# Kernel tuning notes

Hardware: AMD Instinct MI355X
Metric: run time of the kernel (lower is better)

Reference implementation:

```python
import jax, jax.numpy as jnp
import numpy as np

C = 512
GROUPS = 32
EPS = 1e-6


def setup_inputs() -> dict:
    key = jax.random.key(0)
    ks = jax.random.split(key, 6)
    B, L = 8, 2048
    x = jax.random.normal(ks[0], (B, C, L), dtype=jnp.float32)
    # fan_avg variance-scaling uniform for 1x1 conv weights [C, C]
    bound = float(np.sqrt(3.0 / C))  # fan_in == fan_out == C for 1x1 conv
    Wq = jax.random.uniform(ks[1], (C, C), jnp.float32, -bound, bound)
    Wk = jax.random.uniform(ks[2], (C, C), jnp.float32, -bound, bound)
    Wv = jax.random.uniform(ks[3], (C, C), jnp.float32, -bound, bound)
    # proj_out uses init_scale=0.0 (gain 1e-10) -> effectively zeros; use tiny
    bound0 = float(np.sqrt(3.0 * 1e-10 / C))
    Wp = jax.random.uniform(ks[4], (C, C), jnp.float32, -bound0, bound0)
    bq = jnp.zeros((C,), jnp.float32)
    bk = jnp.zeros((C,), jnp.float32)
    bv = jnp.zeros((C,), jnp.float32)
    bp = jnp.zeros((C,), jnp.float32)
    gamma = jnp.ones((C,), jnp.float32)
    beta = jnp.zeros((C,), jnp.float32)
    return {"x": x, "Wq": Wq, "bq": bq, "Wk": Wk, "bk": bk,
            "Wv": Wv, "bv": bv, "Wp": Wp, "bp": bp,
            "gamma": gamma, "beta": beta}


def _group_norm(x, gamma, beta):
    # x: [B, C, L]
    B, Cc, L = x.shape
    xg = x.reshape(B, GROUPS, Cc // GROUPS, L)
    mean = jnp.mean(xg, axis=(2, 3), keepdims=True)
    var = jnp.var(xg, axis=(2, 3), keepdims=True)
    xn = ((xg - mean) * jax.lax.rsqrt(var + EPS)).reshape(B, Cc, L)
    return xn * gamma[None, :, None] + beta[None, :, None]


def reference(x, Wq, bq, Wk, bk, Wv, bv, Wp, bp, gamma, beta):
    h = _group_norm(x, gamma, beta)
    # 1x1 convs are channel-mixing matmuls: out[b,o,l] = W[o,c] h[b,c,l] + b[o]
    q = jnp.einsum('oc,bcl->bol', Wq, h) + bq[None, :, None]
    k = jnp.einsum('oc,bcl->bol', Wk, h) + bk[None, :, None]
    v = jnp.einsum('oc,bcl->bol', Wv, h) + bv[None, :, None]
    scale = float(x.shape[1]) ** (-0.5)
    attn = jnp.einsum('bcl,bcm->blm', q, k) * scale  # [B, L, L]
    attn = jax.nn.softmax(attn, axis=-1)
    h2 = jnp.einsum('bcm,blm->bcl', v, attn)
    h2 = jnp.einsum('oc,bcl->bol', Wp, h2) + bp[None, :, None]
    return x + h2
```

## Files before the change

kernel.cpp:

```cpp
#include <hip/hip_runtime.h>
#include <cstdint>

#define B_DIM 8
#define C_DIM 512
#define L_DIM 2048
#define NGROUPS 32
#define CPG 16
#define EPSV 1e-6f

typedef unsigned short u16;
typedef unsigned int u32;
typedef __attribute__((ext_vector_type(4))) float f32x4;
typedef __attribute__((ext_vector_type(8))) short bf16x8;
typedef const __attribute__((address_space(1))) char gchar;
typedef __attribute__((address_space(3))) char lchar;

__device__ __forceinline__ u16 f2bf(float f) {
  u32 u = __float_as_uint(f);
  u = (u + 0x7fffu + ((u >> 16) & 1u)) >> 16;
  return (u16)u;
}
__device__ __forceinline__ float bf2f(u16 h) {
  return __uint_as_float(((u32)h) << 16);
}

__global__ __launch_bounds__(256) void f2bf_k(const float* __restrict__ in,
                                              u16* __restrict__ out, int n4) {
  int i = blockIdx.x * 256 + threadIdx.x;
  if (i >= n4) return;
  float4 v = ((const float4*)in)[i];
  int2 o;
  o.x = (int)((u32)f2bf(v.x) | ((u32)f2bf(v.y) << 16));
  o.y = (int)((u32)f2bf(v.z) | ((u32)f2bf(v.w) << 16));
  ((int2*)out)[i] = o;
}

__global__ __launch_bounds__(256) void bias_cat_k(const float* __restrict__ a,
                                                  const float* __restrict__ b,
                                                  float* __restrict__ o) {
  int i = blockIdx.x * 256 + threadIdx.x;
  if (i < C_DIM) o[i] = a[i];
  else if (i < 2 * C_DIM) o[i] = b[i - C_DIM];
}

__global__ __launch_bounds__(256) void gn_stats_k(const float* __restrict__ x,
                                                  float* __restrict__ meanp,
                                                  float* __restrict__ rstdp) {
  const int bg = blockIdx.x;
  const float4* xv = (const float4*)(x + (size_t)bg * CPG * L_DIM);
  const int tid = threadIdx.x;
  float s = 0.f, ss = 0.f;
  for (int i = tid; i < CPG * L_DIM / 4; i += 256) {
    float4 v = xv[i];
    s += v.x + v.y + v.z + v.w;
    ss += v.x * v.x + v.y * v.y + v.z * v.z + v.w * v.w;
  }
#pragma unroll
  for (int o = 32; o > 0; o >>= 1) {
    s += __shfl_down(s, o);
    ss += __shfl_down(ss, o);
  }
  __shared__ float r1[4], r2[4];
  if ((tid & 63) == 0) { r1[tid >> 6] = s; r2[tid >> 6] = ss; }
  __syncthreads();
  if (tid == 0) {
    float S = r1[0] + r1[1] + r1[2] + r1[3];
    float SS = r2[0] + r2[1] + r2[2] + r2[3];
    const float invn = 1.f / (CPG * L_DIM);
    float mu = S * invn;
    float var = SS * invn - mu * mu;
    meanp[bg] = mu;
    rstdp[bg] = rsqrtf(var + EPSV);
  }
}

__global__ __launch_bounds__(256) void gn_apply_k(
    const float* __restrict__ x, const float* __restrict__ meanp,
    const float* __restrict__ rstdp, const float* __restrict__ gamma,
    const float* __restrict__ beta, u16* __restrict__ hT) {
  __shared__ float sm[64][65];
  const int b = blockIdx.z, c0 = blockIdx.y * 64, l0 = blockIdx.x * 64;
  const int tid = threadIdx.x;
#pragma unroll
  for (int p = 0; p < 4; ++p) {
    int cc = p * 16 + (tid >> 4);
    int ll = (tid & 15) * 4;
    float4 v = *(const float4*)(x + ((size_t)b * C_DIM + c0 + cc) * L_DIM + l0 + ll);
    int grp = (c0 + cc) >> 4;
    float rs = rstdp[b * NGROUPS + grp];
    float ga = gamma[c0 + cc] * rs;
    float be = beta[c0 + cc] - meanp[b * NGROUPS + grp] * ga;
    sm[cc][ll + 0] = v.x * ga + be;
    sm[cc][ll + 1] = v.y * ga + be;
    sm[cc][ll + 2] = v.z * ga + be;
    sm[cc][ll + 3] = v.w * ga + be;
  }
  __syncthreads();
#pragma unroll
  for (int i = 0; i < 8; ++i) {
    int w = tid + 256 * i;
    int ll = w >> 5;
    int cw = (w & 31) * 2;
    u32 pk = (u32)f2bf(sm[cw][ll]) | ((u32)f2bf(sm[cw + 1][ll]) << 16);
    *(u32*)(hT + ((size_t)b * L_DIM + l0 + ll) * C_DIM + c0 + cw) = pk;
  }
}

__global__ __launch_bounds__(256) void softmax_k(u16* __restrict__ S) {
  const int tid = threadIdx.x;
  u16* row = S + (size_t)blockIdx.x * L_DIM;
  union { int4 v; u16 u[8]; } in;
  in.v = ((const int4*)row)[tid];
  float f[8];
#pragma unroll
  for (int j = 0; j < 8; ++j) f[j] = bf2f(in.u[j]);
  float mx = f[0];
#pragma unroll
  for (int j = 1; j < 8; ++j) mx = fmaxf(mx, f[j]);
#pragma unroll
  for (int o = 32; o > 0; o >>= 1) mx = fmaxf(mx, __shfl_down(mx, o));
  __shared__ float r1[4], r2[4];
  if ((tid & 63) == 0) r1[tid >> 6] = mx;
  __syncthreads();
  mx = fmaxf(fmaxf(r1[0], r1[1]), fmaxf(r1[2], r1[3]));
  float s = 0.f;
#pragma unroll
  for (int j = 0; j < 8; ++j) { f[j] = __expf(f[j] - mx); s += f[j]; }
#pragma unroll
  for (int o = 32; o > 0; o >>= 1) s += __shfl_down(s, o);
  if ((tid & 63) == 0) r2[tid >> 6] = s;
  __syncthreads();
  float inv = 1.f / (r2[0] + r2[1] + r2[2] + r2[3]);
  union { int4 v; u16 u[8]; } outp;
#pragma unroll
  for (int j = 0; j < 8; ++j) outp.u[j] = f2bf(f[j] * inv);
  ((int4*)row)[tid] = outp.v;
}

template <int MODE>
__global__ __launch_bounds__(256, 4) void gemm_tn(
    const u16* __restrict__ A, long sA, long lda,
    const u16* __restrict__ Bp, long sB, long ldb,
    void* __restrict__ Cv, long sC, int M, int N, int K,
    const float* __restrict__ bias, const float* __restrict__ Xres, long sX,
    float scale) {
  constexpr int BM = 128, BN = 128, BK = 64;
  __shared__ u16 smem[2 * BM * BK];
  u16* As = smem;
  u16* Bs = smem + BM * BK;
  const int bz = blockIdx.z;
  A += (long)bz * sA;
  Bp += (long)bz * sB;
  const int m0 = blockIdx.x * BM;
  const int n0 = blockIdx.y * BN;
  const int tid = threadIdx.x;
  const int lane = tid & 63;
  const int wid = tid >> 6;
  const int wr = wid >> 1, wc = wid & 1;

  f32x4 acc[4][4] = {};

  const int srow = wid * 32 + (lane >> 3);
  const int scolb = ((lane & 7) << 4) ^ (((lane >> 3) & 7) << 4);
  auto stage = [&](int k0) {
#pragma unroll
    for (int q = 0; q < 4; ++q) {
      int seg = wid * 4 + q;
      int row = srow + q * 8;
      const char* ga = (const char*)A + ((long)(m0 + row) * lda + k0) * 2 + scolb;
      __builtin_amdgcn_global_load_lds((gchar*)ga,
                                       (lchar*)((char*)As + seg * 1024), 16, 0, 0);
      const char* gb = (const char*)Bp + ((long)(n0 + row) * ldb + k0) * 2 + scolb;
      __builtin_amdgcn_global_load_lds((gchar*)gb,
                                       (lchar*)((char*)Bs + seg * 1024), 16, 0, 0);
    }
  };

  const int nkt = K / BK;
  stage(0);
  for (int kt = 0; kt < nkt; ++kt) {
    __syncthreads();
#pragma unroll
    for (int ks = 0; ks < 2; ++ks) {
      bf16x8 af[4], bfv[4];
#pragma unroll
      for (int f = 0; f < 4; ++f) {
        int ra = wr * 64 + f * 16 + (lane & 15);
        int oa = (ra * 128 + ks * 64 + ((lane >> 4) * 16)) ^ ((ra & 7) << 4);
        af[f] = *(const bf16x8*)((const char*)As + oa);
        int rb = wc * 64 + f * 16 + (lane & 15);
        int ob = (rb * 128 + ks * 64 + ((lane >> 4) * 16)) ^ ((rb & 7) << 4);
        bfv[f] = *(const bf16x8*)((const char*)Bs + ob);
      }
#pragma unroll
      for (int i = 0; i < 4; ++i)
#pragma unroll
        for (int j = 0; j < 4; ++j)
          acc[i][j] = __builtin_amdgcn_mfma_f32_16x16x32_bf16(af[i], bfv[j],
                                                              acc[i][j], 0, 0, 0);
    }
    if (kt + 1 < nkt) {
      __syncthreads();
      stage((kt + 1) * BK);
    }
  }

  const int mb = wr * 64 + ((lane >> 4) << 2);
  const int nb = wc * 64 + (lane & 15);
  if (MODE == 4) {
#pragma unroll
    for (int i = 0; i < 4; ++i)
#pragma unroll
      for (int j = 0; j < 4; ++j)
#pragma unroll
        for (int r = 0; r < 4; ++r) {
          int m = m0 + mb + i * 16 + r;
          int n = n0 + nb + j * 16;
          long off = (long)m * N + n;
          ((float*)Cv)[(long)bz * sC + off] =
              acc[i][j][r] + bias[m] + Xres[(long)bz * sX + off];
        }
  } else {
    __syncthreads();
    u16* Cs = smem;
#pragma unroll
    for (int i = 0; i < 4; ++i)
#pragma unroll
      for (int j = 0; j < 4; ++j)
#pragma unroll
        for (int r = 0; r < 4; ++r) {
          float val = acc[i][j][r];
          int ml = mb + i * 16 + r;
          int nl = nb + j * 16;
          if (MODE == 0) val += bias[n0 + nl];
          if (MODE == 1) val += bias[m0 + ml];
          if (MODE == 2) val *= scale;
          int byt = (ml * 256 + nl * 2) ^ ((ml & 7) << 4);
          *(u16*)((char*)Cs + byt) = f2bf(val);
        }
    __syncthreads();
#pragma unroll
    for (int u = 0; u < 8; ++u) {
      int c = u * 256 + tid;
      int row = c >> 4, c4 = c & 15;
      int lb = (row * 256 + c4 * 16) ^ ((row & 7) << 4);
      int4 vv = *(const int4*)((const char*)Cs + lb);
      *(int4*)((u16*)Cv + (long)bz * sC + (long)(m0 + row) * N + n0 + c4 * 8) = vv;
    }
  }
}

extern "C" void kernel_launch(void* const* d_in, const int* in_sizes, int n_in,
                              void* d_out, int out_size, void* d_ws,
                              size_t ws_size, hipStream_t stream) {
  const float* x = (const float*)d_in[0];
  const float* Wq = (const float*)d_in[1];
  const float* bq = (const float*)d_in[2];
  const float* Wk = (const float*)d_in[3];
  const float* bk = (const float*)d_in[4];
  const float* Wv = (const float*)d_in[5];
  const float* bv = (const float*)d_in[6];
  const float* Wp = (const float*)d_in[7];
  const float* bp = (const float*)d_in[8];
  const float* gamma = (const float*)d_in[9];
  const float* beta = (const float*)d_in[10];
  float* out = (float*)d_out;

  const size_t BLC = (size_t)B_DIM * L_DIM * C_DIM;
  const size_t BLL = (size_t)B_DIM * L_DIM * L_DIM;
  const int CC = C_DIM * C_DIM;
  u16* vbuf = (u16*)d_ws;
  u16* qkT = vbuf + BLC;
  u16* Sbuf = qkT + 2 * BLC;
  u16* hT = Sbuf;
  u16* h2T = qkT;
  u16* wqkb = Sbuf + BLL;
  u16* wvb = wqkb + 2 * CC;
  u16* wpb = wvb + CC;
  float* meanp = (float*)(wpb + CC);
  float* rstdp = meanp + B_DIM * NGROUPS;
  float* bqk = rstdp + B_DIM * NGROUPS;

  const long LC = (long)L_DIM * C_DIM;
  const long CL = (long)C_DIM * L_DIM;
  const long LL = (long)L_DIM * L_DIM;
  const long LQK = (long)L_DIM * 2 * C_DIM;
  const float scale = 1.0f / sqrtf((float)C_DIM);

  f2bf_k<<<256, 256, 0, stream>>>(Wq, wqkb, CC / 4);
  f2bf_k<<<256, 256, 0, stream>>>(Wk, wqkb + CC, CC / 4);
  f2bf_k<<<256, 256, 0, stream>>>(Wv, wvb, CC / 4);
  f2bf_k<<<256, 256, 0, stream>>>(Wp, wpb, CC / 4);
  bias_cat_k<<<4, 256, 0, stream>>>(bq, bk, bqk);
  gn_stats_k<<<B_DIM * NGROUPS, 256, 0, stream>>>(x, meanp, rstdp);
  gn_apply_k<<<dim3(L_DIM / 64, C_DIM / 64, B_DIM), 256, 0, stream>>>(
      x, meanp, rstdp, gamma, beta, hT);
  gemm_tn<0><<<dim3(L_DIM / 128, 2 * C_DIM / 128, B_DIM), 256, 0, stream>>>(
      hT, LC, C_DIM, wqkb, 0L, C_DIM, qkT, LQK, L_DIM, 2 * C_DIM, C_DIM,
      bqk, nullptr, 0L, 0.f);
  gemm_tn<1><<<dim3(C_DIM / 128, L_DIM / 128, B_DIM), 256, 0, stream>>>(
      wvb, 0L, C_DIM, hT, LC, C_DIM, vbuf, CL, C_DIM, L_DIM, C_DIM,
      bv, nullptr, 0L, 0.f);
  gemm_tn<2><<<dim3(L_DIM / 128, L_DIM / 128, B_DIM), 256, 0, stream>>>(
      qkT, LQK, 2 * C_DIM, qkT + C_DIM, LQK, 2 * C_DIM, Sbuf, LL,
      L_DIM, L_DIM, C_DIM, nullptr, nullptr, 0L, scale);
  softmax_k<<<B_DIM * L_DIM, 256, 0, stream>>>(Sbuf);
  gemm_tn<3><<<dim3(L_DIM / 128, C_DIM / 128, B_DIM), 256, 0, stream>>>(
      Sbuf, LL, L_DIM, vbuf, CL, L_DIM, h2T, LC, L_DIM, C_DIM, L_DIM,
      nullptr, nullptr, 0L, 0.f);
  gemm_tn<4><<<dim3(C_DIM / 128, L_DIM / 128, B_DIM), 256, 0, stream>>>(
      wpb, 0L, C_DIM, h2T, LC, C_DIM, out, CL, C_DIM, L_DIM, C_DIM,
      bp, x, CL, 0.f);
}
```

Before: 287.1 us.

## Double-buffer GEMM LDS staging, use wave-per-row softmax, merge prep kernels

The GEMM now keeps two LDS buffers and issues the next k-tile's global-to-LDS loads before computing the current tile, with one barrier per iteration instead of two. This is meant to overlap memory latency with MFMA work, at the cost of doubling LDS to 64KB per block, which may reduce occupancy below the launch_bounds target of 4 blocks. Softmax now gives each 64-lane wave a full row and reduces with shuffles only, removing shared memory and block barriers. The four weight-conversion launches and the bias concat are merged into one kernel to cut launch overhead.

```diff
diff --git a/kernel.cpp b/kernel.cpp
--- a/kernel.cpp
+++ b/kernel.cpp
@@ -24,23 +24,30 @@
   return __uint_as_float(((u32)h) << 16);
 }
 
-__global__ __launch_bounds__(256) void f2bf_k(const float* __restrict__ in,
-                                              u16* __restrict__ out, int n4) {
-  int i = blockIdx.x * 256 + threadIdx.x;
-  if (i >= n4) return;
-  float4 v = ((const float4*)in)[i];
-  int2 o;
-  o.x = (int)((u32)f2bf(v.x) | ((u32)f2bf(v.y) << 16));
-  o.y = (int)((u32)f2bf(v.z) | ((u32)f2bf(v.w) << 16));
-  ((int2*)out)[i] = o;
-}
-
-__global__ __launch_bounds__(256) void bias_cat_k(const float* __restrict__ a,
-                                                  const float* __restrict__ b,
-                                                  float* __restrict__ o) {
-  int i = blockIdx.x * 256 + threadIdx.x;
-  if (i < C_DIM) o[i] = a[i];
-  else if (i < 2 * C_DIM) o[i] = b[i - C_DIM];
+__global__ __launch_bounds__(256) void prep_k(
+    const float* __restrict__ Wq, const float* __restrict__ Wk,
+    const float* __restrict__ Wv, const float* __restrict__ Wp,
+    const float* __restrict__ bq, const float* __restrict__ bk,
+    u16* __restrict__ wqkb, u16* __restrict__ wvb, u16* __restrict__ wpb,
+    float* __restrict__ bqk) {
+  const int g = blockIdx.x;
+  if (g < 1024) {
+    const int w = g >> 8;
+    const float* src = w == 0 ? Wq : w == 1 ? Wk : w == 2 ? Wv : Wp;
+    u16* dst = w == 0 ? wqkb : w == 1 ? wqkb + C_DIM * C_DIM : w == 2 ? wvb : wpb;
+    int i = (g & 255) * 256 + threadIdx.x;
+    float4 v = ((const float4*)src)[i];
+    int2 o;
+    o.x = (int)((u32)f2bf(v.x) | ((u32)f2bf(v.y) << 16));
+    o.y = (int)((u32)f2bf(v.z) | ((u32)f2bf(v.w) << 16));
+    ((int2*)dst)[i] = o;
+  } else {
+#pragma unroll
+    for (int q = 0; q < 4; ++q) {
+      int idx = q * 256 + threadIdx.x;
+      bqk[idx] = idx < C_DIM ? bq[idx] : bk[idx - C_DIM];
+    }
+  }
 }
 
 __global__ __launch_bounds__(256) void gn_stats_k(const float* __restrict__ x,
@@ -107,34 +114,34 @@
 }
 
 __global__ __launch_bounds__(256) void softmax_k(u16* __restrict__ S) {
-  const int tid = threadIdx.x;
-  u16* row = S + (size_t)blockIdx.x * L_DIM;
-  union { int4 v; u16 u[8]; } in;
-  in.v = ((const int4*)row)[tid];
-  float f[8];
-#pragma unroll
-  for (int j = 0; j < 8; ++j) f[j] = bf2f(in.u[j]);
+  const int lane = threadIdx.x & 63;
+  const size_t row = (size_t)blockIdx.x * 4 + (threadIdx.x >> 6);
+  u16* r = S + row * L_DIM;
+  float f[32];
+  union { int4 v; u16 u[8]; } cv;
+#pragma unroll
+  for (int q = 0; q < 4; ++q) {
+    cv.v = ((const int4*)r)[q * 64 + lane];
+#pragma unroll
+    for (int j = 0; j < 8; ++j) f[q * 8 + j] = bf2f(cv.u[j]);
+  }
   float mx = f[0];
 #pragma unroll
-  for (int j = 1; j < 8; ++j) mx = fmaxf(mx, f[j]);
-#pragma unroll
-  for (int o = 32; o > 0; o >>= 1) mx = fmaxf(mx, __shfl_down(mx, o));
-  __shared__ float r1[4], r2[4];
-  if ((tid & 63) == 0) r1[tid >> 6] = mx;
-  __syncthreads();
-  mx = fmaxf(fmaxf(r1[0], r1[1]), fmaxf(r1[2], r1[3]));
+  for (int j = 1; j < 32; ++j) mx = fmaxf(mx, f[j]);
+#pragma unroll
+  for (int o = 1; o < 64; o <<= 1) mx = fmaxf(mx, __shfl_xor(mx, o));
   float s = 0.f;
 #pragma unroll
-  for (int j = 0; j < 8; ++j) { f[j] = __expf(f[j] - mx); s += f[j]; }
-#pragma unroll
-  for (int o = 32; o > 0; o >>= 1) s += __shfl_down(s, o);
-  if ((tid & 63) == 0) r2[tid >> 6] = s;
-  __syncthreads();
-  float inv = 1.f / (r2[0] + r2[1] + r2[2] + r2[3]);
-  union { int4 v; u16 u[8]; } outp;
-#pragma unroll
-  for (int j = 0; j < 8; ++j) outp.u[j] = f2bf(f[j] * inv);
-  ((int4*)row)[tid] = outp.v;
+  for (int j = 0; j < 32; ++j) { f[j] = __expf(f[j] - mx); s += f[j]; }
+#pragma unroll
+  for (int o = 1; o < 64; o <<= 1) s += __shfl_xor(s, o);
+  float inv = 1.f / s;
+#pragma unroll
+  for (int q = 0; q < 4; ++q) {
+#pragma unroll
+    for (int j = 0; j < 8; ++j) cv.u[j] = f2bf(f[q * 8 + j] * inv);
+    ((int4*)r)[q * 64 + lane] = cv.v;
+  }
 }
 
 template <int MODE>
@@ -145,9 +152,7 @@
     const float* __restrict__ bias, const float* __restrict__ Xres, long sX,
     float scale) {
   constexpr int BM = 128, BN = 128, BK = 64;
-  __shared__ u16 smem[2 * BM * BK];
-  u16* As = smem;
-  u16* Bs = smem + BM * BK;
+  __shared__ u16 smem[2][2 * BM * BK];
   const int bz = blockIdx.z;
   A += (long)bz * sA;
   Bp += (long)bz * sB;
@@ -162,7 +167,9 @@
 
   const int srow = wid * 32 + (lane >> 3);
   const int scolb = ((lane & 7) << 4) ^ (((lane >> 3) & 7) << 4);
-  auto stage = [&](int k0) {
+  auto stage = [&](int k0, int buf) {
+    u16* As = smem[buf];
+    u16* Bs = smem[buf] + BM * BK;
 #pragma unroll
     for (int q = 0; q < 4; ++q) {
       int seg = wid * 4 + q;
@@ -177,9 +184,13 @@
   };
 
   const int nkt = K / BK;
-  stage(0);
+  stage(0, 0);
+  int cur = 0;
   for (int kt = 0; kt < nkt; ++kt) {
     __syncthreads();
+    if (kt + 1 < nkt) stage((kt + 1) * BK, cur ^ 1);
+    const u16* As = smem[cur];
+    const u16* Bs = smem[cur] + BM * BK;
 #pragma unroll
     for (int ks = 0; ks < 2; ++ks) {
       bf16x8 af[4], bfv[4];
@@ -199,10 +210,7 @@
           acc[i][j] = __builtin_amdgcn_mfma_f32_16x16x32_bf16(af[i], bfv[j],
                                                               acc[i][j], 0, 0, 0);
     }
-    if (kt + 1 < nkt) {
-      __syncthreads();
-      stage((kt + 1) * BK);
-    }
+    cur ^= 1;
   }
 
   const int mb = wr * 64 + ((lane >> 4) << 2);
@@ -222,7 +230,7 @@
         }
   } else {
     __syncthreads();
-    u16* Cs = smem;
+    u16* Cs = smem[0];
 #pragma unroll
     for (int i = 0; i < 4; ++i)
 #pragma unroll
@@ -287,11 +295,7 @@
   const long LQK = (long)L_DIM * 2 * C_DIM;
   const float scale = 1.0f / sqrtf((float)C_DIM);
 
-  f2bf_k<<<256, 256, 0, stream>>>(Wq, wqkb, CC / 4);
-  f2bf_k<<<256, 256, 0, stream>>>(Wk, wqkb + CC, CC / 4);
-  f2bf_k<<<256, 256, 0, stream>>>(Wv, wvb, CC / 4);
-  f2bf_k<<<256, 256, 0, stream>>>(Wp, wpb, CC / 4);
-  bias_cat_k<<<4, 256, 0, stream>>>(bq, bk, bqk);
+  prep_k<<<1025, 256, 0, stream>>>(Wq, Wk, Wv, Wp, bq, bk, wqkb, wvb, wpb, bqk);
   gn_stats_k<<<B_DIM * NGROUPS, 256, 0, stream>>>(x, meanp, rstdp);
   gn_apply_k<<<dim3(L_DIM / 64, C_DIM / 64, B_DIM), 256, 0, stream>>>(
       x, meanp, rstdp, gamma, beta, hT);
@@ -304,7 +308,7 @@
   gemm_tn<2><<<dim3(L_DIM / 128, L_DIM / 128, B_DIM), 256, 0, stream>>>(
       qkT, LQK, 2 * C_DIM, qkT + C_DIM, LQK, 2 * C_DIM, Sbuf, LL,
       L_DIM, L_DIM, C_DIM, nullptr, nullptr, 0L, scale);
-  softmax_k<<<B_DIM * L_DIM, 256, 0, stream>>>(Sbuf);
+  softmax_k<<<B_DIM * L_DIM / 4, 256, 0, stream>>>(Sbuf);
   gemm_tn<3><<<dim3(L_DIM / 128, C_DIM / 128, B_DIM), 256, 0, stream>>>(
       Sbuf, LL, L_DIM, vbuf, CL, L_DIM, h2T, LC, L_DIM, C_DIM, L_DIM,
       nullptr, nullptr, 0L, 0.f);
```

Measured after the change: 303.6 us. +5.7%, slower.
